# Kernel tuning notes

Measured on AMD Instinct MI355X. Metric: run time of the kernel, lower is better.

## Reference

```python
import jax, jax.numpy as jnp
import numpy as np

N_NODES = 100000
N_EDGES = 1600000
IN_SIZE, HID_SIZE, OUT_SIZE = 128, 64, 64


def _glorot(key, shape):
    lim = float(np.sqrt(6.0 / (shape[0] + shape[1])))
    return jax.random.uniform(key, shape, jnp.float32, -lim, lim)


def setup_inputs() -> dict:
    key = jax.random.key(0)
    ks = jax.random.split(key, 6)
    features = jax.random.normal(ks[0], (N_NODES, IN_SIZE), jnp.float32)
    src = jax.random.randint(ks[1], (N_EDGES,), 0, N_NODES)
    dst = jax.random.randint(ks[2], (N_EDGES,), 0, N_NODES)
    return {
        "features": features,
        "W0": _glorot(ks[3], (IN_SIZE, HID_SIZE)),
        "b0": jnp.zeros((HID_SIZE,), jnp.float32),
        "W1": _glorot(ks[4], (HID_SIZE, HID_SIZE)),
        "b1": jnp.zeros((HID_SIZE,), jnp.float32),
        "W2": _glorot(ks[5], (HID_SIZE, OUT_SIZE)),
        "b2": jnp.zeros((OUT_SIZE,), jnp.float32),
        "src": src,
        "dst": dst,
    }


def reference(features, W0, b0, W1, b1, W2, b2, src, dst):
    # DGL GraphConv with norm='both': h' = relu(D_in^{-1/2} A D_out^{-1/2} h W + b)
    # Dropout layers are identity in eval mode (deterministic baseline).
    N = features.shape[0]
    ones = jnp.ones(src.shape, features.dtype)
    deg_out = jax.ops.segment_sum(ones, src, num_segments=N)
    deg_in = jax.ops.segment_sum(ones, dst, num_segments=N)
    norm_src = jnp.where(deg_out > 0, deg_out, 1.0) ** -0.5  # [N]
    norm_dst = jnp.where(deg_in > 0, deg_in, 1.0) ** -0.5    # [N]

    def layer(h, W, b):
        h = h * norm_src[:, None]          # source-side degree norm
        m = (h @ W)[src]                   # project first (in >= out), then gather [E, d_out]
        agg = jax.ops.segment_sum(m, dst, num_segments=N)  # scatter-add to destinations
        return jax.nn.relu(agg * norm_dst[:, None] + b)

    h = layer(features, W0, b0)
    h = layer(h, W1, b1)
    return layer(h, W2, b2)
```

## Files before the change

kernel.cpp:

```cpp
#include <hip/hip_runtime.h>
#include <hip/hip_bf16.h>

typedef __hip_bfloat16 bf16;
typedef __attribute__((ext_vector_type(8))) short bf16x8;
typedef __attribute__((ext_vector_type(8))) unsigned short u16x8;
typedef __attribute__((ext_vector_type(4))) float f32x4;
typedef __attribute__((ext_vector_type(4))) int i32x4;
typedef __attribute__((ext_vector_type(4))) short s16x4;

__device__ __forceinline__ float b2f(unsigned short u) {
  return __uint_as_float(((unsigned)u) << 16);
}
__device__ __forceinline__ unsigned short f2b(float x) {
  bf16 h = __float2bfloat16(x);
  return *reinterpret_cast<unsigned short*>(&h);
}

__global__ void k_passA(const int* __restrict__ src, const int* __restrict__ dst, int E,
                        int nbuck, int M, int* __restrict__ counts,
                        const unsigned short* __restrict__ raw, int* __restrict__ flag) {
  if (blockIdx.x == 256) {
    __shared__ int sbad, snz;
    const int t = threadIdx.x;
    if (t == 0) { sbad = 0; snz = 0; }
    __syncthreads();
    const unsigned short u = raw[t];
    const float a = fabsf(b2f(u));
    if (!(a < 100.f)) atomicAdd(&sbad, 1);
    if (((t & 1) == 0) && u != 0) atomicAdd(&snz, 1);
    __syncthreads();
    if (t == 0) flag[0] = (sbad == 0 && snz > 0) ? 1 : 0;
    return;
  }
  extern __shared__ int lh[];
  int* lh1 = lh;
  int* lh2 = lh + nbuck;
  const int t = threadIdx.x;
  for (int k = t; k < 2 * nbuck; k += 256) lh[k] = 0;
  __syncthreads();
  const int chunk = (E + 255) / 256;
  const int s = blockIdx.x * chunk;
  const int e = min(E, s + chunk);
  for (int i = s + t; i < e; i += 256) {
    atomicAdd(&lh1[dst[i] >> 8], 1);
    atomicAdd(&lh2[src[i] >> 8], 1);
  }
  __syncthreads();
  for (int k = t; k < nbuck; k += 256) {
    counts[k * 256 + blockIdx.x] = lh1[k];
    counts[M + k * 256 + blockIdx.x] = lh2[k];
  }
}

__global__ void k_scan1(const int* __restrict__ a, int M2, int* __restrict__ bsums) {
  __shared__ int sdata[256];
  int i = blockIdx.x * 256 + threadIdx.x;
  int v = (i < M2) ? a[i] : 0;
  sdata[threadIdx.x] = v;
  __syncthreads();
  for (int s = 128; s > 0; s >>= 1) {
    if (threadIdx.x < s) sdata[threadIdx.x] += sdata[threadIdx.x + s];
    __syncthreads();
  }
  if (threadIdx.x == 0) bsums[blockIdx.x] = sdata[0];
}

__global__ void k_scan2(int* __restrict__ bsums, int nb, int* __restrict__ rowStart,
                        int N, int E) {
  __shared__ int s[1024];
  const int t = threadIdx.x;
  const int v = (t < nb) ? bsums[t] : 0;
  s[t] = v;
  __syncthreads();
  for (int off = 1; off < 1024; off <<= 1) {
    int u = (t >= off) ? s[t - off] : 0;
    __syncthreads();
    s[t] += u;
    __syncthreads();
  }
  if (t < nb) bsums[t] = s[t] - v;
  if (t == 0) rowStart[N] = E;
}

__global__ void k_scan3(int* __restrict__ a, int M2, const int* __restrict__ bsums) {
  __shared__ int sdata[256];
  int i = blockIdx.x * 256 + threadIdx.x;
  int v = (i < M2) ? a[i] : 0;
  sdata[threadIdx.x] = v;
  __syncthreads();
  for (int off = 1; off < 256; off <<= 1) {
    int t = (threadIdx.x >= off) ? sdata[threadIdx.x - off] : 0;
    __syncthreads();
    sdata[threadIdx.x] += t;
    __syncthreads();
  }
  if (i < M2) a[i] = bsums[blockIdx.x] + sdata[threadIdx.x] - v;
}

__global__ void k_passC(const int* __restrict__ src, const int* __restrict__ dst, int E,
                        int nbuck, int M, const int* __restrict__ S,
                        int* __restrict__ tmp, unsigned char* __restrict__ tmp2) {
  extern __shared__ int cur[];
  int* cur1 = cur;
  int* cur2 = cur + nbuck;
  const int t = threadIdx.x;
  for (int k = t; k < nbuck; k += 256) {
    cur1[k] = S[k * 256 + blockIdx.x];
    cur2[k] = S[M + k * 256 + blockIdx.x];
  }
  __syncthreads();
  const int chunk = (E + 255) / 256;
  const int s = blockIdx.x * chunk;
  const int e = min(E, s + chunk);
  for (int i = s + t; i < e; i += 256) {
    const int sv = src[i];
    const int d = dst[i];
    const int pos1 = atomicAdd(&cur1[d >> 8], 1);
    tmp[pos1] = sv | ((d & 255) << 20);
    const int pos2 = atomicAdd(&cur2[sv >> 8], 1);
    tmp2[pos2 - E] = (unsigned char)(sv & 255);
  }
}

__global__ void k_passD(const int* __restrict__ tmp, const unsigned char* __restrict__ tmp2,
                        const int* __restrict__ S, int nbuck, int M, int N, int E,
                        int* __restrict__ rowStart, int* __restrict__ edgeSrc,
                        float* __restrict__ ns, float* __restrict__ nd) {
  __shared__ int h[256];
  __shared__ int ex[256];
  __shared__ int c[256];
  const int t = threadIdx.x;
  const int k = blockIdx.x;
  const int node = k * 256 + t;
  const int bs2 = S[M + k * 256] - E;
  const int be2 = (k + 1 < nbuck) ? (S[M + (k + 1) * 256] - E) : E;
  h[t] = 0;
  __syncthreads();
  for (int i = bs2 + t; i < be2; i += 256) atomicAdd(&h[tmp2[i]], 1);
  __syncthreads();
  if (node < N) {
    int dov = h[t];
    if (dov <= 0) dov = 1;
    ns[node] = rsqrtf((float)dov);
  }
  __syncthreads();
  const int bs = S[k * 256];
  const int be = (k + 1 < nbuck) ? S[(k + 1) * 256] : E;
  h[t] = 0;
  __syncthreads();
  for (int i = bs + t; i < be; i += 256) atomicAdd(&h[tmp[i] >> 20], 1);
  __syncthreads();
  const int cnt = h[t];
  ex[t] = cnt;
  __syncthreads();
  for (int off = 1; off < 256; off <<= 1) {
    int u = (t >= off) ? ex[t - off] : 0;
    __syncthreads();
    ex[t] += u;
    __syncthreads();
  }
  const int excl = ex[t] - cnt;
  if (node < N) {
    rowStart[node] = bs + excl;
    nd[node] = rsqrtf((float)(cnt > 0 ? cnt : 1));
  }
  c[t] = bs + excl;
  __syncthreads();
  for (int i = bs + t; i < be; i += 256) {
    const int v = tmp[i];
    const int pos = atomicAdd(&c[v >> 20], 1);
    edgeSrc[pos] = v & 0xFFFFF;
  }
}

template <int K, bool FIRST, bool SCALE>
__global__ void __launch_bounds__(256) k_gemm(
    const void* __restrict__ hin, const void* __restrict__ Wv,
    const int* __restrict__ flag, const float* __restrict__ norm_src,
    int N, unsigned short* __restrict__ out) {
  constexpr int ST = K + 8;
  constexpr int CST = 72;
  __shared__ unsigned short Wl[64 * ST];
  __shared__ unsigned short Cl[4][16 * CST];
  const bool isb = (*flag != 0);
  const int tid = threadIdx.x;

  {
    const unsigned short* Wus = (const unsigned short*)Wv;
    const float* Wf = (const float*)Wv;
    for (int i0 = tid * 8; i0 < K * 64; i0 += 2048) {
      const int k = i0 >> 6;
      const int n0 = i0 & 63;
      unsigned short v[8];
      if (isb) {
        const u16x8 u = *(const u16x8*)(Wus + i0);
#pragma unroll
        for (int j = 0; j < 8; ++j) v[j] = u[j];
      } else {
        const float4 f0 = *(const float4*)(Wf + i0);
        const float4 f1 = *(const float4*)(Wf + i0 + 4);
        v[0] = f2b(f0.x); v[1] = f2b(f0.y); v[2] = f2b(f0.z); v[3] = f2b(f0.w);
        v[4] = f2b(f1.x); v[5] = f2b(f1.y); v[6] = f2b(f1.z); v[7] = f2b(f1.w);
      }
#pragma unroll
      for (int j = 0; j < 8; ++j) Wl[(n0 + j) * ST + k] = v[j];
    }
  }
  __syncthreads();

  const int lane = tid & 63;
  const int quad = lane >> 4;
  const int l16 = lane & 15;
  const int w = tid >> 6;
  unsigned short* myC = &Cl[w][0];

  const int wid = blockIdx.x * 4 + w;
  const int nw = gridDim.x * 4;
  const int G = (N + 15) >> 4;
  constexpr int KT = K / 32;

  for (int g = wid; g < G; g += nw) {
    int rowA = (g << 4) + l16;
    if (rowA >= N) rowA = N - 1;
    f32x4 acc[4] = {{0.f, 0.f, 0.f, 0.f}, {0.f, 0.f, 0.f, 0.f},
                    {0.f, 0.f, 0.f, 0.f}, {0.f, 0.f, 0.f, 0.f}};
#pragma unroll
    for (int kt = 0; kt < KT; ++kt) {
      const int koff = kt * 32 + quad * 8;
      bf16x8 Af;
      if (FIRST && !isb) {
        const float* hp = (const float*)hin + (size_t)rowA * K + koff;
        const float4 u0 = *(const float4*)hp;
        const float4 u1 = *(const float4*)(hp + 4);
        Af[0] = (short)f2b(u0.x); Af[1] = (short)f2b(u0.y);
        Af[2] = (short)f2b(u0.z); Af[3] = (short)f2b(u0.w);
        Af[4] = (short)f2b(u1.x); Af[5] = (short)f2b(u1.y);
        Af[6] = (short)f2b(u1.z); Af[7] = (short)f2b(u1.w);
      } else {
        Af = *(const bf16x8*)((const unsigned short*)hin + (size_t)rowA * K + koff);
      }
#pragma unroll
      for (int nt = 0; nt < 4; ++nt) {
        const bf16x8 Bf = *(const bf16x8*)&Wl[(nt * 16 + l16) * ST + koff];
        acc[nt] = __builtin_amdgcn_mfma_f32_16x16x32_bf16(Af, Bf, acc[nt], 0, 0, 0);
      }
    }
    const int rowD = quad * 4;
#pragma unroll
    for (int r = 0; r < 4; ++r) {
      const int nodeW = (g << 4) + rowD + r;
      const float f = (SCALE && nodeW < N) ? norm_src[nodeW] : 1.0f;
#pragma unroll
      for (int nt = 0; nt < 4; ++nt)
        myC[(rowD + r) * CST + nt * 16 + l16] = f2b(SCALE ? acc[nt][r] * f : acc[nt][r]);
    }
    const int row2 = lane >> 2;
    const int c0 = (lane & 3) * 16;
    const int node = (g << 4) + row2;
    if (node < N) {
      const u16x8 v0 = *(const u16x8*)&myC[row2 * CST + c0];
      const u16x8 v1 = *(const u16x8*)&myC[row2 * CST + c0 + 8];
      *(u16x8*)(out + (size_t)node * 64 + c0) = v0;
      *(u16x8*)(out + (size_t)node * 64 + c0 + 8) = v1;
    }
  }
}

__device__ __forceinline__ void agg_chunk_compute(unsigned trbase, int cb32, int lo,
                                                  unsigned span, int quad, f32x4* acc) {
  const int posbase = cb32 + (quad << 2);
  const unsigned u0 = (unsigned)(posbase - lo);
  bf16x8 Af;
#pragma unroll
  for (int j = 0; j < 8; ++j) {
    const unsigned off = (j < 4) ? (unsigned)j : (unsigned)(12 + j);
    Af[j] = ((u0 + off) < span) ? (short)0x3F80 : (short)0;
  }
  s16x4 t0[4], t1[4];
#pragma unroll
  for (int nt = 0; nt < 4; ++nt) {
    const unsigned a = trbase + (unsigned)(nt * 1024);
    asm volatile("ds_read_b64_tr_b16 %0, %1" : "=v"(t0[nt]) : "v"(a) : "memory");
    asm volatile("ds_read_b64_tr_b16 %0, %1 offset:512" : "=v"(t1[nt]) : "v"(a) : "memory");
  }
  asm volatile("s_waitcnt lgkmcnt(0)" ::: "memory");
  __builtin_amdgcn_sched_barrier(0);
#pragma unroll
  for (int nt = 0; nt < 4; ++nt) {
    bf16x8 Bf;
    Bf[0] = t0[nt][0]; Bf[1] = t0[nt][1]; Bf[2] = t0[nt][2]; Bf[3] = t0[nt][3];
    Bf[4] = t1[nt][0]; Bf[5] = t1[nt][1]; Bf[6] = t1[nt][2]; Bf[7] = t1[nt][3];
    acc[nt] = __builtin_amdgcn_mfma_f32_16x16x32_bf16(Af, Bf, acc[nt], 0, 0, 0);
  }
}

template <bool LAST>
__global__ void __launch_bounds__(256) k_aggregate(
    const unsigned short* __restrict__ proj,
    const int* __restrict__ edgeSrc, const int* __restrict__ rowStart,
    const float* __restrict__ norm_dst, const float* __restrict__ norm_src,
    const void* __restrict__ bias, const int* __restrict__ flag,
    int N, int E, void* __restrict__ outp) {
  __shared__ unsigned short lds[4][2048];
  const bool isb = (*flag != 0);
  const int tid = threadIdx.x;
  const int w = tid >> 6;
  const int lane = tid & 63;
  const int l16 = lane & 15;
  const int quad = lane >> 4;
  const int e32 = lane & 31;
  const int p = lane >> 5;

  const int wid = blockIdx.x * 4 + w;
  const int g0 = wid * 8;

  float bcol[4];
#pragma unroll
  for (int nt = 0; nt < 4; ++nt) {
    const int col = nt * 16 + l16;
    bcol[nt] = isb ? b2f(((const unsigned short*)bias)[col]) : ((const float*)bias)[col];
  }

  const int cb = rowStart[min(g0, N)];
  const int ce = rowStart[min(g0 + 8, N)];
  const int L = ce - cb;
  const int nch = (L + 31) >> 5;

  const int rsi = min(g0 + min(l16, 8), N);
  const int rsj = min(g0 + min(l16 + 1, 8), N);
  const int lo = rowStart[rsi];
  const unsigned span = (unsigned)(rowStart[rsj] - lo);

  int idxc[6];
#pragma unroll
  for (int t = 0; t < 6; ++t) {
    const int pos = min(cb + t * 32 + e32, E - 1);
    idxc[t] = edgeSrc[pos];
  }

  unsigned short* myl = &lds[w][0];
  unsigned wofs[4];
#pragma unroll
  for (int q = 0; q < 4; ++q) {
    const int n0 = p * 32 + q * 8;
    wofs[q] = (unsigned)((n0 >> 4) * 512 + e32 * 16 + (n0 & 15));
  }
  const unsigned trbase = (unsigned)(uintptr_t)myl + (unsigned)lane * 8u;

  f32x4 acc[4] = {{0.f, 0.f, 0.f, 0.f}, {0.f, 0.f, 0.f, 0.f},
                  {0.f, 0.f, 0.f, 0.f}, {0.f, 0.f, 0.f, 0.f}};

  i32x4 gb[2][4];
#define AGG_ISSUE(t, b)                                                         \
  {                                                                             \
    const unsigned short* rp = proj + (size_t)idxc[t] * 64 + p * 32;            \
    gb[b][0] = *(const i32x4*)(rp);                                             \
    gb[b][1] = *(const i32x4*)(rp + 8);                                         \
    gb[b][2] = *(const i32x4*)(rp + 16);                                        \
    gb[b][3] = *(const i32x4*)(rp + 24);                                        \
  }
  if (0 < nch) AGG_ISSUE(0, 0);
  if (1 < nch) AGG_ISSUE(1, 1);

#pragma unroll
  for (int tt = 0; tt < 6; ++tt) {
    if (tt < nch) {
#pragma unroll
      for (int q = 0; q < 4; ++q) *(i32x4*)(myl + wofs[q]) = gb[tt & 1][q];
      if (tt + 2 < 6 && tt + 2 < nch) AGG_ISSUE(tt + 2, tt & 1);
      asm volatile("s_waitcnt lgkmcnt(0)" ::: "memory");
      agg_chunk_compute(trbase, cb + tt * 32, lo, span, quad, acc);
    }
  }
  for (int t = 6; t < nch; ++t) {
    const int pos = min(cb + t * 32 + e32, E - 1);
    const int idx = edgeSrc[pos];
    const unsigned short* rp = proj + (size_t)idx * 64 + p * 32;
    i32x4 g4[4];
    g4[0] = *(const i32x4*)(rp);
    g4[1] = *(const i32x4*)(rp + 8);
    g4[2] = *(const i32x4*)(rp + 16);
    g4[3] = *(const i32x4*)(rp + 24);
#pragma unroll
    for (int q = 0; q < 4; ++q) *(i32x4*)(myl + wofs[q]) = g4[q];
    asm volatile("s_waitcnt lgkmcnt(0)" ::: "memory");
    agg_chunk_compute(trbase, cb + t * 32, lo, span, quad, acc);
  }
#undef AGG_ISSUE

#pragma unroll
  for (int reg = 0; reg < 4; ++reg) {
    const int row = quad * 4 + reg;
    const int node = g0 + row;
    if (row < 8 && node < N) {
      const float nd = norm_dst[node];
      const float esc = LAST ? 1.f : norm_src[node];
#pragma unroll
      for (int nt = 0; nt < 4; ++nt) {
        float x = fmaxf(fmaf(acc[nt][reg], nd, bcol[nt]), 0.f);
        if (!LAST) x *= esc;
        const size_t o = (size_t)node * 64 + nt * 16 + l16;
        if (LAST && !isb)
          ((float*)outp)[o] = x;
        else
          ((unsigned short*)outp)[o] = f2b(x);
      }
    }
  }
}

extern "C" void kernel_launch(void* const* d_in, const int* in_sizes, int n_in,
                              void* d_out, int out_size, void* d_ws, size_t ws_size,
                              hipStream_t stream) {
  const void* features = d_in[0];
  const void* W0 = d_in[1];
  const void* b0 = d_in[2];
  const void* W1 = d_in[3];
  const void* b1 = d_in[4];
  const void* W2 = d_in[5];
  const void* b2 = d_in[6];
  const int* src = (const int*)d_in[7];
  const int* dst = (const int*)d_in[8];
  const int N = in_sizes[0] / 128;
  const int E = in_sizes[7];
  const int NBUCK = (N + 255) >> 8;
  const int M = NBUCK * 256;
  const int M2 = 2 * M;

  char* w = (char*)d_ws;
  size_t off = 0;
  auto alloc = [&](size_t bytes) {
    void* p = w + off;
    off = (off + bytes + 255) & ~(size_t)255;
    return p;
  };
  int* flag = (int*)alloc(4);
  int* rowStart = (int*)alloc((size_t)(N + 1) * 4);
  int* counts = (int*)alloc((size_t)M2 * 4);
  int* bsums = (int*)alloc(1024 * 4);
  float* norm_src = (float*)alloc((size_t)N * 4);
  float* norm_dst = (float*)alloc((size_t)N * 4);
  int* tmp = (int*)alloc((size_t)E * 4);
  unsigned char* tmp2 = (unsigned char*)alloc((size_t)E);
  int* edgeSrc = (int*)alloc((size_t)E * 4);
  unsigned short* projA = (unsigned short*)alloc((size_t)N * 64 * 2);
  unsigned short* hB = (unsigned short*)d_out;

  const size_t lds_nb = (size_t)NBUCK * 2 * 4;
  const int GB = 1024;

  k_passA<<<257, 256, lds_nb, stream>>>(src, dst, E, NBUCK, M, counts,
                                        (const unsigned short*)features, flag);
  const int NB2 = (M2 + 255) / 256;
  k_scan1<<<NB2, 256, 0, stream>>>(counts, M2, bsums);
  k_scan2<<<1, 1024, 0, stream>>>(bsums, NB2, rowStart, N, E);
  k_scan3<<<NB2, 256, 0, stream>>>(counts, M2, bsums);
  k_passC<<<256, 256, lds_nb, stream>>>(src, dst, E, NBUCK, M, counts, tmp, tmp2);
  k_passD<<<NBUCK, 256, 0, stream>>>(tmp, tmp2, counts, NBUCK, M, N, E,
                                     rowStart, edgeSrc, norm_src, norm_dst);

  const int AB = (((N + 7) / 8) + 3) / 4;
  k_gemm<128, true, true><<<GB, 256, 0, stream>>>(features, W0, flag, norm_src, N, projA);
  k_aggregate<false><<<AB, 256, 0, stream>>>(projA, edgeSrc, rowStart, norm_dst, norm_src, b0, flag, N, E, hB);
  k_gemm<64, false, false><<<GB, 256, 0, stream>>>(hB, W1, flag, nullptr, N, projA);
  k_aggregate<false><<<AB, 256, 0, stream>>>(projA, edgeSrc, rowStart, norm_dst, norm_src, b1, flag, N, E, hB);
  k_gemm<64, false, false><<<GB, 256, 0, stream>>>(hB, W2, flag, nullptr, N, projA);
  k_aggregate<true><<<AB, 256, 0, stream>>>(projA, edgeSrc, rowStart, norm_dst, norm_src, b2, flag, N, E, d_out);
}
```

Baseline: 312.0 us.

## Pre-transpose weights, register-resident B, prefetch A rows, deeper gather pipeline, staged stores

```diff
diff --git a/kernel.cpp b/kernel.cpp
--- a/kernel.cpp
+++ b/kernel.cpp
@@ -173,77 +173,101 @@
   }
 }
 
+__global__ void k_prepW(const void* __restrict__ W0, const void* __restrict__ W1,
+                        const void* __restrict__ W2, const int* __restrict__ flag,
+                        unsigned short* __restrict__ WT0, unsigned short* __restrict__ WT1,
+                        unsigned short* __restrict__ WT2) {
+  const bool isb = (*flag != 0);
+  const int i = blockIdx.x * 256 + threadIdx.x;
+  if (i < 8192) {
+    const int n = i >> 7, k = i & 127;
+    const float v = isb ? b2f(((const unsigned short*)W0)[k * 64 + n])
+                        : ((const float*)W0)[k * 64 + n];
+    WT0[i] = f2b(v);
+  } else if (i < 12288) {
+    const int j = i - 8192;
+    const int n = j >> 6, k = j & 63;
+    const float v = isb ? b2f(((const unsigned short*)W1)[k * 64 + n])
+                        : ((const float*)W1)[k * 64 + n];
+    WT1[j] = f2b(v);
+  } else if (i < 16384) {
+    const int j = i - 12288;
+    const int n = j >> 6, k = j & 63;
+    const float v = isb ? b2f(((const unsigned short*)W2)[k * 64 + n])
+                        : ((const float*)W2)[k * 64 + n];
+    WT2[j] = f2b(v);
+  }
+}
+
+template <int K, bool FIRST, bool SCALE>
+__device__ __forceinline__ void gemm_loadA(const void* hin, bool isb, int rowA,
+                                           int quad, bf16x8* A) {
+  constexpr int KT = K / 32;
+  if (FIRST && !isb) {
+    const float* hp = (const float*)hin + (size_t)rowA * K;
+#pragma unroll
+    for (int kt = 0; kt < KT; ++kt) {
+      const float4 u0 = *(const float4*)(hp + kt * 32 + quad * 8);
+      const float4 u1 = *(const float4*)(hp + kt * 32 + quad * 8 + 4);
+      A[kt][0] = (short)f2b(u0.x); A[kt][1] = (short)f2b(u0.y);
+      A[kt][2] = (short)f2b(u0.z); A[kt][3] = (short)f2b(u0.w);
+      A[kt][4] = (short)f2b(u1.x); A[kt][5] = (short)f2b(u1.y);
+      A[kt][6] = (short)f2b(u1.z); A[kt][7] = (short)f2b(u1.w);
+    }
+  } else {
+    const unsigned short* hp = (const unsigned short*)hin + (size_t)rowA * K;
+#pragma unroll
+    for (int kt = 0; kt < KT; ++kt)
+      A[kt] = *(const bf16x8*)(hp + kt * 32 + quad * 8);
+  }
+}
+
 template <int K, bool FIRST, bool SCALE>
 __global__ void __launch_bounds__(256) k_gemm(
-    const void* __restrict__ hin, const void* __restrict__ Wv,
+    const void* __restrict__ hin, const unsigned short* __restrict__ WT,
     const int* __restrict__ flag, const float* __restrict__ norm_src,
     int N, unsigned short* __restrict__ out) {
-  constexpr int ST = K + 8;
+  constexpr int KT = K / 32;
   constexpr int CST = 72;
-  __shared__ unsigned short Wl[64 * ST];
   __shared__ unsigned short Cl[4][16 * CST];
   const bool isb = (*flag != 0);
   const int tid = threadIdx.x;
-
-  {
-    const unsigned short* Wus = (const unsigned short*)Wv;
-    const float* Wf = (const float*)Wv;
-    for (int i0 = tid * 8; i0 < K * 64; i0 += 2048) {
-      const int k = i0 >> 6;
-      const int n0 = i0 & 63;
-      unsigned short v[8];
-      if (isb) {
-        const u16x8 u = *(const u16x8*)(Wus + i0);
-#pragma unroll
-        for (int j = 0; j < 8; ++j) v[j] = u[j];
-      } else {
-        const float4 f0 = *(const float4*)(Wf + i0);
-        const float4 f1 = *(const float4*)(Wf + i0 + 4);
-        v[0] = f2b(f0.x); v[1] = f2b(f0.y); v[2] = f2b(f0.z); v[3] = f2b(f0.w);
-        v[4] = f2b(f1.x); v[5] = f2b(f1.y); v[6] = f2b(f1.z); v[7] = f2b(f1.w);
-      }
-#pragma unroll
-      for (int j = 0; j < 8; ++j) Wl[(n0 + j) * ST + k] = v[j];
-    }
-  }
-  __syncthreads();
-
   const int lane = tid & 63;
   const int quad = lane >> 4;
   const int l16 = lane & 15;
   const int w = tid >> 6;
   unsigned short* myC = &Cl[w][0];
 
+  bf16x8 Bf[KT][4];
+#pragma unroll
+  for (int kt = 0; kt < KT; ++kt)
+#pragma unroll
+    for (int nt = 0; nt < 4; ++nt)
+      Bf[kt][nt] = *(const bf16x8*)(WT + (size_t)(nt * 16 + l16) * K + kt * 32 + quad * 8);
+
   const int wid = blockIdx.x * 4 + w;
   const int nw = gridDim.x * 4;
   const int G = (N + 15) >> 4;
-  constexpr int KT = K / 32;
-
+
+  bf16x8 A0[KT], A1[KT];
+  if (wid < G) {
+    int r0 = (wid << 4) + l16;
+    if (r0 >= N) r0 = N - 1;
+    gemm_loadA<K, FIRST, SCALE>(hin, isb, r0, quad, A0);
+  }
   for (int g = wid; g < G; g += nw) {
-    int rowA = (g << 4) + l16;
-    if (rowA >= N) rowA = N - 1;
+    if (g + nw < G) {
+      int r1 = ((g + nw) << 4) + l16;
+      if (r1 >= N) r1 = N - 1;
+      gemm_loadA<K, FIRST, SCALE>(hin, isb, r1, quad, A1);
+    }
     f32x4 acc[4] = {{0.f, 0.f, 0.f, 0.f}, {0.f, 0.f, 0.f, 0.f},
                     {0.f, 0.f, 0.f, 0.f}, {0.f, 0.f, 0.f, 0.f}};
 #pragma unroll
     for (int kt = 0; kt < KT; ++kt) {
-      const int koff = kt * 32 + quad * 8;
-      bf16x8 Af;
-      if (FIRST && !isb) {
-        const float* hp = (const float*)hin + (size_t)rowA * K + koff;
-        const float4 u0 = *(const float4*)hp;
-        const float4 u1 = *(const float4*)(hp + 4);
-        Af[0] = (short)f2b(u0.x); Af[1] = (short)f2b(u0.y);
-        Af[2] = (short)f2b(u0.z); Af[3] = (short)f2b(u0.w);
-        Af[4] = (short)f2b(u1.x); Af[5] = (short)f2b(u1.y);
-        Af[6] = (short)f2b(u1.z); Af[7] = (short)f2b(u1.w);
-      } else {
-        Af = *(const bf16x8*)((const unsigned short*)hin + (size_t)rowA * K + koff);
-      }
-#pragma unroll
-      for (int nt = 0; nt < 4; ++nt) {
-        const bf16x8 Bf = *(const bf16x8*)&Wl[(nt * 16 + l16) * ST + koff];
-        acc[nt] = __builtin_amdgcn_mfma_f32_16x16x32_bf16(Af, Bf, acc[nt], 0, 0, 0);
-      }
+#pragma unroll
+      for (int nt = 0; nt < 4; ++nt)
+        acc[nt] = __builtin_amdgcn_mfma_f32_16x16x32_bf16(A0[kt], Bf[kt][nt], acc[nt], 0, 0, 0);
     }
     const int rowD = quad * 4;
 #pragma unroll
@@ -263,6 +287,8 @@
       *(u16x8*)(out + (size_t)node * 64 + c0) = v0;
       *(u16x8*)(out + (size_t)node * 64 + c0 + 8) = v1;
     }
+#pragma unroll
+    for (int kt = 0; kt < KT; ++kt) A0[kt] = A1[kt];
   }
 }
 
@@ -350,7 +376,7 @@
   f32x4 acc[4] = {{0.f, 0.f, 0.f, 0.f}, {0.f, 0.f, 0.f, 0.f},
                   {0.f, 0.f, 0.f, 0.f}, {0.f, 0.f, 0.f, 0.f}};
 
-  i32x4 gb[2][4];
+  i32x4 gb[4][4];
 #define AGG_ISSUE(t, b)                                                         \
   {                                                                             \
     const unsigned short* rp = proj + (size_t)idxc[t] * 64 + p * 32;            \
@@ -361,13 +387,15 @@
   }
   if (0 < nch) AGG_ISSUE(0, 0);
   if (1 < nch) AGG_ISSUE(1, 1);
+  if (2 < nch) AGG_ISSUE(2, 2);
+  if (3 < nch) AGG_ISSUE(3, 3);
 
 #pragma unroll
   for (int tt = 0; tt < 6; ++tt) {
     if (tt < nch) {
 #pragma unroll
-      for (int q = 0; q < 4; ++q) *(i32x4*)(myl + wofs[q]) = gb[tt & 1][q];
-      if (tt + 2 < 6 && tt + 2 < nch) AGG_ISSUE(tt + 2, tt & 1);
+      for (int q = 0; q < 4; ++q) *(i32x4*)(myl + wofs[q]) = gb[tt & 3][q];
+      if (tt + 4 < 6 && tt + 4 < nch) AGG_ISSUE(tt + 4, tt & 3);
       asm volatile("s_waitcnt lgkmcnt(0)" ::: "memory");
       agg_chunk_compute(trbase, cb + tt * 32, lo, span, quad, acc);
     }
@@ -388,22 +416,58 @@
   }
 #undef AGG_ISSUE
 
-#pragma unroll
-  for (int reg = 0; reg < 4; ++reg) {
-    const int row = quad * 4 + reg;
-    const int node = g0 + row;
-    if (row < 8 && node < N) {
-      const float nd = norm_dst[node];
-      const float esc = LAST ? 1.f : norm_src[node];
-#pragma unroll
-      for (int nt = 0; nt < 4; ++nt) {
-        float x = fmaxf(fmaf(acc[nt][reg], nd, bcol[nt]), 0.f);
-        if (!LAST) x *= esc;
-        const size_t o = (size_t)node * 64 + nt * 16 + l16;
-        if (LAST && !isb)
-          ((float*)outp)[o] = x;
-        else
-          ((unsigned short*)outp)[o] = f2b(x);
+  if (LAST && !isb) {
+    float* fs = (float*)myl;
+#pragma unroll
+    for (int reg = 0; reg < 4; ++reg) {
+      const int row = quad * 4 + reg;
+      if (row < 8) {
+        const int node = min(g0 + row, N - 1);
+        const float nd = norm_dst[node];
+#pragma unroll
+        for (int nt = 0; nt < 4; ++nt)
+          fs[row * 64 + nt * 16 + l16] = fmaxf(fmaf(acc[nt][reg], nd, bcol[nt]), 0.f);
+      }
+    }
+    asm volatile("s_waitcnt lgkmcnt(0)" ::: "memory");
+    __builtin_amdgcn_sched_barrier(0);
+    const int r = lane >> 3;
+    const int c0 = (lane & 7) * 8;
+    const int node = g0 + r;
+    if (node < N) {
+      const float4 v0 = *(const float4*)&fs[r * 64 + c0];
+      const float4 v1 = *(const float4*)&fs[r * 64 + c0 + 4];
+      float* of = (float*)outp + (size_t)node * 64 + c0;
+      *(float4*)of = v0;
+      *(float4*)(of + 4) = v1;
+    }
+  } else {
+#pragma unroll
+    for (int reg = 0; reg < 4; ++reg) {
+      const int row = quad * 4 + reg;
+      if (row < 8) {
+        const int node = min(g0 + row, N - 1);
+        const float nd = norm_dst[node];
+        const float esc = LAST ? 1.f : norm_src[node];
+#pragma unroll
+        for (int nt = 0; nt < 4; ++nt) {
+          float x = fmaxf(fmaf(acc[nt][reg], nd, bcol[nt]), 0.f);
+          if (!LAST) x *= esc;
+          myl[row * 64 + nt * 16 + l16] = f2b(x);
+        }
+      }
+    }
+    asm volatile("s_waitcnt lgkmcnt(0)" ::: "memory");
+    __builtin_amdgcn_sched_barrier(0);
+    if (lane < 32) {
+      const int r = lane >> 2;
+      const int c0 = (lane & 3) * 16;
+      const int node = g0 + r;
+      if (node < N) {
+        const u16x8 v0 = *(const u16x8*)&myl[r * 64 + c0];
+        const u16x8 v1 = *(const u16x8*)&myl[r * 64 + c0 + 8];
+        *(u16x8*)((unsigned short*)outp + (size_t)node * 64 + c0) = v0;
+        *(u16x8*)((unsigned short*)outp + (size_t)node * 64 + c0 + 8) = v1;
       }
     }
   }
@@ -444,10 +508,14 @@
   unsigned char* tmp2 = (unsigned char*)alloc((size_t)E);
   int* edgeSrc = (int*)alloc((size_t)E * 4);
   unsigned short* projA = (unsigned short*)alloc((size_t)N * 64 * 2);
+  unsigned short* WT0 = (unsigned short*)alloc(64 * 128 * 2);
+  unsigned short* WT1 = (unsigned short*)alloc(64 * 64 * 2);
+  unsigned short* WT2 = (unsigned short*)alloc(64 * 64 * 2);
   unsigned short* hB = (unsigned short*)d_out;
 
   const size_t lds_nb = (size_t)NBUCK * 2 * 4;
-  const int GB = 1024;
+  const int G16 = (N + 15) / 16;
+  const int GB = (G16 + 7) / 8;
 
   k_passA<<<257, 256, lds_nb, stream>>>(src, dst, E, NBUCK, M, counts,
                                         (const unsigned short*)features, flag);
@@ -458,12 +526,13 @@
   k_passC<<<256, 256, lds_nb, stream>>>(src, dst, E, NBUCK, M, counts, tmp, tmp2);
   k_passD<<<NBUCK, 256, 0, stream>>>(tmp, tmp2, counts, NBUCK, M, N, E,
                                      rowStart, edgeSrc, norm_src, norm_dst);
+  k_prepW<<<64, 256, 0, stream>>>(W0, W1, W2, flag, WT0, WT1, WT2);
 
   const int AB = (((N + 7) / 8) + 3) / 4;
-  k_gemm<128, true, true><<<GB, 256, 0, stream>>>(features, W0, flag, norm_src, N, projA);
+  k_gemm<128, true, true><<<GB, 256, 0, stream>>>(features, WT0, flag, norm_src, N, projA);
   k_aggregate<false><<<AB, 256, 0, stream>>>(projA, edgeSrc, rowStart, norm_dst, norm_src, b0, flag, N, E, hB);
-  k_gemm<64, false, false><<<GB, 256, 0, stream>>>(hB, W1, flag, nullptr, N, projA);
+  k_gemm<64, false, false><<<GB, 256, 0, stream>>>(hB, WT1, flag, nullptr, N, projA);
   k_aggregate<false><<<AB, 256, 0, stream>>>(projA, edgeSrc, rowStart, norm_dst, norm_src, b1, flag, N, E, hB);
-  k_gemm<64, false, false><<<GB, 256, 0, stream>>>(hB, W2, flag, nullptr, N, projA);
+  k_gemm<64, false, false><<<GB, 256, 0, stream>>>(hB, WT2, flag, nullptr, N, projA);
   k_aggregate<true><<<AB, 256, 0, stream>>>(projA, edgeSrc, rowStart, norm_dst, norm_src, b2, flag, N, E, d_out);
 }
```

Result: slower. 335.3 us (+7.5%).
